# Performance work log

Hardware: AMD Instinct MI355X
Metric: run time of the kernel (lower is better)

## Reference

```python
import jax, jax.numpy as jnp
import numpy as np

H = 8  # attention_heads


def _ln(x, w, b, eps=1e-5):
    mu = x.mean(axis=-1, keepdims=True)
    var = x.var(axis=-1, keepdims=True)
    return (x - mu) / jnp.sqrt(var + eps) * w + b


def setup_inputs() -> dict:
    key = jax.random.key(0)
    ks = jax.random.split(key, 10)
    B, T, C, U, D, P = 4, 256, 2048, 4, 512, 512
    s = 0.02
    inp = {
        "model_embed": jax.random.normal(ks[0], (B, T, D), jnp.float32),
        "context_embed_key": jax.random.normal(ks[1], (C, U, D), jnp.float32),
        "context_embed_value": jax.random.normal(ks[2], (C, D), jnp.float32),
        "ln1_w": jnp.ones((D,), jnp.float32), "ln1_b": jnp.zeros((D,), jnp.float32),
        "ln2_w": jnp.ones((D,), jnp.float32), "ln2_b": jnp.zeros((D,), jnp.float32),
        "ln3_w": jnp.ones((D,), jnp.float32), "ln3_b": jnp.zeros((D,), jnp.float32),
        "ln4_w": jnp.ones((D,), jnp.float32), "ln4_b": jnp.zeros((D,), jnp.float32),
        "wq": jax.random.normal(ks[3], (D, D), jnp.float32) * s, "bq": jnp.zeros((D,), jnp.float32),
        "wk": jax.random.normal(ks[4], (D, D), jnp.float32) * s, "bk": jnp.zeros((D,), jnp.float32),
        "wv": jax.random.normal(ks[5], (D, D), jnp.float32) * s, "bv": jnp.zeros((D,), jnp.float32),
        "wo": jax.random.normal(ks[6], (D, D), jnp.float32) * s, "bo": jnp.zeros((D,), jnp.float32),
        "wp": jax.random.normal(ks[7], (D, P), jnp.float32) * s, "bp": jnp.zeros((P,), jnp.float32),
    }
    return inp


def reference(model_embed, context_embed_key, context_embed_value,
              ln1_w, ln1_b, ln2_w, ln2_b, ln3_w, ln3_b, ln4_w, ln4_b,
              wq, bq, wk, bk, wv, bv, wo, bo, wp, bp):
    B, T, D = model_embed.shape
    C, U, _ = context_embed_key.shape
    dk = D // H
    # pre-attention LayerNorms (norm_before_x1/x2/x3)
    q = _ln(model_embed, ln1_w, ln1_b)
    k = _ln(context_embed_key, ln2_w, ln2_b)
    v = _ln(context_embed_value, ln3_w, ln3_b)
    # q/k/v projections, split heads
    q = (q @ wq + bq).reshape(B, T, H, dk)
    k = (k @ wk + bk).reshape(C, U, H, dk)
    v = (v @ wv + bv).reshape(C, H, dk)
    # ColBERT late interaction: score every query token against every
    # context vector, MaxSim over the U vectors of each context entry.
    scores = jnp.einsum('bthd,cuhd->bhtcu', q, k) / jnp.sqrt(jnp.asarray(dk, q.dtype))
    scores = scores.max(axis=-1)                 # [B,H,T,C]
    attn = jax.nn.softmax(scores, axis=-1)       # softmax over contexts C
    out = jnp.einsum('bhtc,chd->bthd', attn, v).reshape(B, T, D)
    out = out @ wo + bo                          # attention output proj
    out = _ln(out, ln4_w, ln4_b)                 # norm_after
    return out @ wp + bp                         # final proj -> [B,T,P]
```

## Files before the change

kernel.cpp:

```cpp
#include <hip/hip_runtime.h>
#include <hip/hip_bf16.h>

using bf16 = __hip_bfloat16;

#define D_DIM 512
#define C_DIM 2048
#define U_DIM 4
#define DK 64

typedef __attribute__((ext_vector_type(8))) short short8;
typedef __attribute__((ext_vector_type(8))) unsigned short ushort8;
typedef __attribute__((ext_vector_type(4))) float f32x4;

__device__ __forceinline__ float dload(const void* p, size_t i, int f) {
    return f ? ((const float*)p)[i] : __bfloat162float(((const bf16*)p)[i]);
}
__device__ __forceinline__ unsigned f2bf(float x) {
    bf16 b = __float2bfloat16(x);
    return (unsigned)*(unsigned short*)&b;
}
__device__ __forceinline__ float bf2f(unsigned short us) {
    unsigned u = ((unsigned)us) << 16;
    return __builtin_bit_cast(float, u);
}

__device__ __forceinline__ int block_detect(const void* __restrict__ x) {
    __shared__ int sred[4];
    const bf16* xb = (const bf16*)x;
    int tid = threadIdx.x;
    int cnt = 0;
    #pragma unroll
    for (int i = 0; i < 4; ++i) {
        ushort8 a = *(const ushort8*)(xb + (size_t)(i * 256 + tid) * 8);
        #pragma unroll
        for (int j = 0; j < 8; ++j) {
            float v = fabsf(bf2f(a[j]));
            if (!(v <= 100.0f)) cnt++;
        }
    }
    #pragma unroll
    for (int o = 32; o > 0; o >>= 1) cnt += __shfl_down(cnt, o);
    if ((tid & 63) == 0) sred[tid >> 6] = cnt;
    __syncthreads();
    int c = sred[0] + sred[1] + sred[2] + sred[3];
    return (c > 400) ? 1 : 0;
}

template <bool LN, bool XF, bool WF>
__device__ __forceinline__ void pack_a_body(const void* __restrict__ X,
                                            const void* __restrict__ lnw,
                                            const void* __restrict__ lnb,
                                            uint4* __restrict__ Af, int tt) {
    int m = threadIdx.x >> 4;
    int kbL = threadIdx.x & 15;
    int row = tt * 16 + m;
    float v[32];
    float s = 0.0f, ss = 0.0f;
    #pragma unroll
    for (int i = 0; i < 4; ++i) {
        int k0 = (kbL + i * 16) * 8;
        if constexpr (XF) {
            const float4* p = (const float4*)((const float*)X + (size_t)row * D_DIM + k0);
            float4 a = p[0], b = p[1];
            v[i*8+0] = a.x; v[i*8+1] = a.y; v[i*8+2] = a.z; v[i*8+3] = a.w;
            v[i*8+4] = b.x; v[i*8+5] = b.y; v[i*8+6] = b.z; v[i*8+7] = b.w;
        } else {
            ushort8 a = *(const ushort8*)((const bf16*)X + (size_t)row * D_DIM + k0);
            #pragma unroll
            for (int j = 0; j < 8; ++j) v[i*8+j] = bf2f(a[j]);
        }
        #pragma unroll
        for (int j = 0; j < 8; ++j) { float x = v[i*8+j]; s += x; ss += x * x; }
    }
    float mu = 0.0f, rs = 1.0f;
    if (LN) {
        #pragma unroll
        for (int o = 1; o < 16; o <<= 1) { s += __shfl_xor(s, o); ss += __shfl_xor(ss, o); }
        mu = s * (1.0f / D_DIM);
        float var = ss * (1.0f / D_DIM) - mu * mu;
        rs = rsqrtf(var + 1e-5f);
    }
    #pragma unroll
    for (int i = 0; i < 4; ++i) {
        int kb = kbL + i * 16;
        int k0 = kb * 8;
        float lw[8], lb[8];
        if (LN) {
            if constexpr (WF) {
                const float4* pw = (const float4*)((const float*)lnw + k0);
                const float4* pb = (const float4*)((const float*)lnb + k0);
                float4 w0 = pw[0], w1 = pw[1], b0 = pb[0], b1 = pb[1];
                lw[0]=w0.x; lw[1]=w0.y; lw[2]=w0.z; lw[3]=w0.w;
                lw[4]=w1.x; lw[5]=w1.y; lw[6]=w1.z; lw[7]=w1.w;
                lb[0]=b0.x; lb[1]=b0.y; lb[2]=b0.z; lb[3]=b0.w;
                lb[4]=b1.x; lb[5]=b1.y; lb[6]=b1.z; lb[7]=b1.w;
            } else {
                ushort8 w8 = *(const ushort8*)((const bf16*)lnw + k0);
                ushort8 b8 = *(const ushort8*)((const bf16*)lnb + k0);
                #pragma unroll
                for (int j = 0; j < 8; ++j) { lw[j] = bf2f(w8[j]); lb[j] = bf2f(b8[j]); }
            }
        }
        unsigned pk[4];
        #pragma unroll
        for (int jp = 0; jp < 4; ++jp) {
            float v0 = v[i * 8 + jp * 2];
            float v1 = v[i * 8 + jp * 2 + 1];
            if (LN) {
                v0 = (v0 - mu) * rs * lw[jp * 2] + lb[jp * 2];
                v1 = (v1 - mu) * rs * lw[jp * 2 + 1] + lb[jp * 2 + 1];
            }
            pk[jp] = f2bf(v0) | (f2bf(v1) << 16);
        }
        uint4 wv = {pk[0], pk[1], pk[2], pk[3]};
        Af[((size_t)tt * 64 + kb) * 16 + m] = wv;
    }
}

template <bool WF>
__device__ __forceinline__ void pack_w_body(const void* __restrict__ W,
                                            uint4* __restrict__ Bf, int b,
                                            float (*t)[65]) {
    int n0 = (b & 7) * 64, k0 = (b >> 3) * 64;
    int tid = threadIdx.x;
    if constexpr (WF) {
        #pragma unroll
        for (int i = 0; i < 4; ++i) {
            int e = i * 256 + tid;
            int r = e >> 4, c = (e & 15) * 4;
            float4 a = *(const float4*)((const float*)W + (size_t)(k0 + r) * D_DIM + n0 + c);
            t[r][c] = a.x; t[r][c+1] = a.y; t[r][c+2] = a.z; t[r][c+3] = a.w;
        }
    } else {
        #pragma unroll
        for (int i = 0; i < 2; ++i) {
            int e = i * 256 + tid;
            int r = e >> 3, c = (e & 7) * 8;
            ushort8 a = *(const ushort8*)((const bf16*)W + (size_t)(k0 + r) * D_DIM + n0 + c);
            #pragma unroll
            for (int j = 0; j < 8; ++j) t[r][c + j] = bf2f(a[j]);
        }
    }
    __syncthreads();
    #pragma unroll
    for (int i = 0; i < 2; ++i) {
        int e = i * 256 + tid;
        int nl = e & 63, kbl = e >> 6;
        unsigned pk[4];
        #pragma unroll
        for (int jp = 0; jp < 4; ++jp)
            pk[jp] = f2bf(t[kbl * 8 + jp * 2][nl]) | (f2bf(t[kbl * 8 + jp * 2 + 1][nl]) << 16);
        uint4 wv = {pk[0], pk[1], pk[2], pk[3]};
        int n = n0 + nl;
        Bf[(((size_t)(n >> 4)) * 64 + (k0 / 8 + kbl)) * 16 + (n & 15)] = wv;
    }
}

__global__ __launch_bounds__(256, 1)
void pack_all_kernel(const void* __restrict__ me, const void* __restrict__ l1w, const void* __restrict__ l1b,
                     const void* __restrict__ ck, const void* __restrict__ l2w, const void* __restrict__ l2b,
                     const void* __restrict__ cv, const void* __restrict__ l3w, const void* __restrict__ l3b,
                     uint4* __restrict__ Aq, uint4* __restrict__ Ak, uint4* __restrict__ Av,
                     const void* W0, const void* W1, const void* W2,
                     const void* W3, const void* W4,
                     uint4* B0, uint4* B1, uint4* B2, uint4* B3, uint4* B4,
                     int* __restrict__ flagp) {
    __shared__ float t[64][65];
    int f = block_detect(me);
    if (blockIdx.x == 0 && threadIdx.x == 0) *flagp = f;
    int b = blockIdx.x;
    const void* Ws[5] = {W0, W1, W2, W3, W4};
    uint4* Bs[5] = {B0, B1, B2, B3, B4};
    if (f) {
        if (b < 64)       pack_a_body<true, true, true>(me, l1w, l1b, Aq, b);
        else if (b < 576) pack_a_body<true, true, true>(ck, l2w, l2b, Ak, b - 64);
        else if (b < 704) pack_a_body<true, true, true>(cv, l3w, l3b, Av, b - 576);
        else { int c = b - 704; pack_w_body<true>(Ws[c >> 6], Bs[c >> 6], c & 63, t); }
    } else {
        if (b < 64)       pack_a_body<true, false, false>(me, l1w, l1b, Aq, b);
        else if (b < 576) pack_a_body<true, false, false>(ck, l2w, l2b, Ak, b - 64);
        else if (b < 704) pack_a_body<true, false, false>(cv, l3w, l3b, Av, b - 576);
        else { int c = b - 704; pack_w_body<false>(Ws[c >> 6], Bs[c >> 6], c & 63, t); }
    }
}

template <int OUT>
__device__ __forceinline__ void mfma_gemm_body(const uint4* __restrict__ Af,
                                               const uint4* __restrict__ Bf,
                                               const void* __restrict__ bias,
                                               uint4* __restrict__ Fout, int Rtt,
                                               int f, int bx, int by,
                                               float (*t)[65]) {
    int w = threadIdx.x >> 6, lane = threadIdx.x & 63;
    int q = lane >> 4, mn = lane & 15;
    int mt = by * 4 + w;
    int nt0 = bx * 4;
    f32x4 acc[4] = {{0.f,0.f,0.f,0.f},{0.f,0.f,0.f,0.f},{0.f,0.f,0.f,0.f},{0.f,0.f,0.f,0.f}};
    for (int kw = 0; kw < 16; ++kw) {
        short8 a = *(const short8*)(Af + ((size_t)mt * 64 + kw * 4 + q) * 16 + mn);
        #pragma unroll
        for (int i = 0; i < 4; ++i) {
            short8 b = *(const short8*)(Bf + (((size_t)(nt0 + i)) * 64 + kw * 4 + q) * 16 + mn);
            acc[i] = __builtin_amdgcn_mfma_f32_16x16x32_bf16(a, b, acc[i], 0, 0, 0);
        }
    }
    #pragma unroll
    for (int i = 0; i < 4; ++i) {
        float bv = dload(bias, (nt0 + i) * 16 + mn, f);
        #pragma unroll
        for (int r = 0; r < 4; ++r)
            t[w * 16 + q * 4 + r][i * 16 + mn] = acc[i][r] + bv;
    }
    __syncthreads();
    int h = bx;
    if constexpr (OUT == 1) {
        #pragma unroll
        for (int e0 = 0; e0 < 2; ++e0) {
            int e = e0 * 256 + threadIdx.x;
            int m = e & 15, kb = (e >> 4) & 7, ttl = e >> 7;
            const float* src = &t[ttl * 16 + m][kb * 8];
            uint4 wv;
            wv.x = f2bf(src[0]) | (f2bf(src[1]) << 16);
            wv.y = f2bf(src[2]) | (f2bf(src[3]) << 16);
            wv.z = f2bf(src[4]) | (f2bf(src[5]) << 16);
            wv.w = f2bf(src[6]) | (f2bf(src[7]) << 16);
            Fout[(((size_t)h * Rtt + by * 4 + ttl) * 8 + kb) * 16 + m] = wv;
        }
    } else if constexpr (OUT == 2) {
        #pragma unroll
        for (int e0 = 0; e0 < 2; ++e0) {
            int e = e0 * 256 + threadIdx.x;
            int lane2 = e & 63, nt = (e >> 6) & 3, ctl = e >> 8;
            int nm2 = lane2 & 15, q2 = lane2 >> 4;
            int col = nt * 16 + nm2;
            int rb = ctl * 32 + q2 * 8;
            uint4 wv;
            wv.x = f2bf(t[rb + 0][col]) | (f2bf(t[rb + 1][col]) << 16);
            wv.y = f2bf(t[rb + 2][col]) | (f2bf(t[rb + 3][col]) << 16);
            wv.z = f2bf(t[rb + 4][col]) | (f2bf(t[rb + 5][col]) << 16);
            wv.w = f2bf(t[rb + 6][col]) | (f2bf(t[rb + 7][col]) << 16);
            Fout[(((size_t)h * 64 + by * 2 + ctl) * 4 + nt) * 64 + lane2] = wv;
        }
    } else {
        #pragma unroll
        for (int e0 = 0; e0 < 2; ++e0) {
            int e = e0 * 256 + threadIdx.x;
            int m2 = e & 15, kb = (e >> 4) & 7, u = e >> 7;
            const float* src = &t[m2 * 4 + u][kb * 8];
            uint4 wv;
            wv.x = f2bf(src[0]) | (f2bf(src[1]) << 16);
            wv.y = f2bf(src[2]) | (f2bf(src[3]) << 16);
            wv.z = f2bf(src[4]) | (f2bf(src[5]) << 16);
            wv.w = f2bf(src[6]) | (f2bf(src[7]) << 16);
            int nt = by * 4 + u;
            Fout[(((size_t)h * 512 + nt) * 8 + kb) * 16 + m2] = wv;
        }
    }
}

__global__ __launch_bounds__(256, 2)
void gemm_qkv_kernel(const uint4* __restrict__ Aq, const uint4* __restrict__ Ak,
                     const uint4* __restrict__ Av,
                     const uint4* __restrict__ wfq, const uint4* __restrict__ wfk,
                     const uint4* __restrict__ wfv,
                     const void* __restrict__ bq, const void* __restrict__ bk,
                     const void* __restrict__ bv,
                     uint4* __restrict__ qf, uint4* __restrict__ kf,
                     uint4* __restrict__ vf,
                     const int* __restrict__ flagp) {
    __shared__ float t[64][65];
    int f = *flagp;
    int b = blockIdx.x;
    if (b < 1024) {
        mfma_gemm_body<3>(Ak, wfk, bk, kf, 512, f, b >> 7, b & 127, t);
    } else if (b < 1280) {
        int c = b - 1024;
        mfma_gemm_body<2>(Av, wfv, bv, vf, 0, f, c >> 5, c & 31, t);
    } else {
        int c = b - 1280;
        mfma_gemm_body<1>(Aq, wfq, bq, qf, 64, f, c >> 4, c & 15, t);
    }
}

__global__ __launch_bounds__(512, 1)
void attn_fused_kernel(const uint4* __restrict__ qf, const uint4* __restrict__ kf,
                       const uint4* __restrict__ vf, uint4* __restrict__ oAf) {
    __shared__ float sp[8][16][36];
    __shared__ float opar[8][16][64];
    __shared__ float mpar[8][16];
    __shared__ float lpar[8][16];
    int tid = threadIdx.x;
    int w = tid >> 6, lane = tid & 63;
    int q = lane >> 4, nm = lane & 15;
    int b = blockIdx.x;
    int h = b & 7;
    int rt = b >> 3;
    int s = w;

    short8 a0 = *(const short8*)(qf + (((size_t)h * 64 + rt) * 8 + q) * 16 + nm);
    short8 a1 = *(const short8*)(qf + (((size_t)h * 64 + rt) * 8 + 4 + q) * 16 + nm);

    f32x4 sc[8][2];
    #pragma unroll
    for (int st = 0; st < 8; ++st) {
        #pragma unroll
        for (int hh = 0; hh < 2; ++hh) {
            int ct16 = (s * 8 + st) * 2 + hh;
            f32x4 scv = {-1e30f, -1e30f, -1e30f, -1e30f};
            __builtin_amdgcn_s_setprio(1);
            #pragma unroll
            for (int u = 0; u < 4; ++u) {
                int nt = ct16 * 4 + u;
                short8 b0 = *(const short8*)(kf + (((size_t)h * 512 + nt) * 8 + q) * 16 + nm);
                short8 b1 = *(const short8*)(kf + (((size_t)h * 512 + nt) * 8 + 4 + q) * 16 + nm);
                f32x4 acc = {0.0f, 0.0f, 0.0f, 0.0f};
                acc = __builtin_amdgcn_mfma_f32_16x16x32_bf16(a0, b0, acc, 0, 0, 0);
                acc = __builtin_amdgcn_mfma_f32_16x16x32_bf16(a1, b1, acc, 0, 0, 0);
                #pragma unroll
                for (int r = 0; r < 4; ++r) scv[r] = fmaxf(scv[r], acc[r]);
            }
            __builtin_amdgcn_s_setprio(0);
            #pragma unroll
            for (int r = 0; r < 4; ++r) sc[st][hh][r] = scv[r] * 0.125f;
        }
    }

    float mrow[4], lrow[4];
    #pragma unroll
    for (int r = 0; r < 4; ++r) {
        float m = sc[0][0][r];
        #pragma unroll
        for (int st = 0; st < 8; ++st) {
            m = fmaxf(m, sc[st][0][r]);
            m = fmaxf(m, sc[st][1][r]);
        }
        m = fmaxf(m, __shfl_xor(m, 1));
        m = fmaxf(m, __shfl_xor(m, 2));
        m = fmaxf(m, __shfl_xor(m, 4));
        m = fmaxf(m, __shfl_xor(m, 8));
        mrow[r] = m;
        lrow[r] = 0.0f;
    }

    f32x4 acc_o[4] = {{0.f,0.f,0.f,0.f},{0.f,0.f,0.f,0.f},{0.f,0.f,0.f,0.f},{0.f,0.f,0.f,0.f}};
    #pragma unroll
    for (int st = 0; st < 8; ++st) {
        #pragma unroll
        for (int r = 0; r < 4; ++r) {
            float p0 = __expf(sc[st][0][r] - mrow[r]);
            float p1 = __expf(sc[st][1][r] - mrow[r]);
            sp[w][q * 4 + r][nm] = p0;
            sp[w][q * 4 + r][16 + nm] = p1;
            lrow[r] += p0 + p1;
        }
        float4 pa0 = *(const float4*)&sp[w][nm][q * 8];
        float4 pa1 = *(const float4*)&sp[w][nm][q * 8 + 4];
        uint4 av;
        av.x = f2bf(pa0.x) | (f2bf(pa0.y) << 16);
        av.y = f2bf(pa0.z) | (f2bf(pa0.w) << 16);
        av.z = f2bf(pa1.x) | (f2bf(pa1.y) << 16);
        av.w = f2bf(pa1.z) | (f2bf(pa1.w) << 16);
        short8 ap = *(short8*)&av;
        int ct32 = s * 8 + st;
        __builtin_amdgcn_s_setprio(1);
        #pragma unroll
        for (int nt2 = 0; nt2 < 4; ++nt2) {
            short8 bv = *(const short8*)(vf + (((size_t)h * 64 + ct32) * 4 + nt2) * 64 + lane);
            acc_o[nt2] = __builtin_amdgcn_mfma_f32_16x16x32_bf16(ap, bv, acc_o[nt2], 0, 0, 0);
        }
        __builtin_amdgcn_s_setprio(0);
    }

    #pragma unroll
    for (int r = 0; r < 4; ++r) {
        float ps = lrow[r];
        ps += __shfl_xor(ps, 1);
        ps += __shfl_xor(ps, 2);
        ps += __shfl_xor(ps, 4);
        ps += __shfl_xor(ps, 8);
        lrow[r] = ps;
    }

    #pragma unroll
    for (int nt2 = 0; nt2 < 4; ++nt2)
        #pragma unroll
        for (int r = 0; r < 4; ++r)
            opar[w][q * 4 + r][nt2 * 16 + nm] = acc_o[nt2][r];
    if (nm == 0) {
        #pragma unroll
        for (int r = 0; r < 4; ++r) {
            mpar[w][q * 4 + r] = mrow[r];
            lpar[w][q * 4 + r] = lrow[r];
        }
    }
    __syncthreads();

    if (tid < 128) {
        int row = tid & 15, dg = tid >> 4;
        float M = -1e30f;
        #pragma unroll
        for (int ss = 0; ss < 8; ++ss) M = fmaxf(M, mpar[ss][row]);
        float L = 0.0f;
        float o[8] = {0.f,0.f,0.f,0.f,0.f,0.f,0.f,0.f};
        #pragma unroll
        for (int ss = 0; ss < 8; ++ss) {
            float e = __expf(mpar[ss][row] - M);
            L += lpar[ss][row] * e;
            const float* po = &opar[ss][row][dg * 8];
            #pragma unroll
            for (int j = 0; j < 8; ++j) o[j] += po[j] * e;
        }
        float inv = 1.0f / L;
        uint4 u;
        u.x = f2bf(o[0] * inv) | (f2bf(o[1] * inv) << 16);
        u.y = f2bf(o[2] * inv) | (f2bf(o[3] * inv) << 16);
        u.z = f2bf(o[4] * inv) | (f2bf(o[5] * inv) << 16);
        u.w = f2bf(o[6] * inv) | (f2bf(o[7] * inv) << 16);
        int kb = h * 8 + dg;
        oAf[((size_t)rt * 64 + kb) * 16 + row] = u;
    }
}

__global__ __launch_bounds__(512, 1)
void tail2_kernel(const uint4* __restrict__ oAf,
                  const uint4* __restrict__ wfo, const uint4* __restrict__ wfp,
                  const void* __restrict__ bo, const void* __restrict__ bp,
                  const void* __restrict__ ln4w, const void* __restrict__ ln4b,
                  float* __restrict__ Y, const int* __restrict__ flagp) {
    __shared__ uint4 lfr[64][16];
    __shared__ float xs[8][16][68];
    __shared__ float lw4[512], lb4[512];
    __shared__ float sred[8][16][2];
    int f = *flagp;
    int tid = threadIdx.x;
    int rt = blockIdx.x;
    if (tid < 512) { lw4[tid] = dload(ln4w, tid, f); lb4[tid] = dload(ln4b, tid, f); }

    int w = tid >> 6, lane = tid & 63;
    int q = lane >> 4, mn = lane & 15;

    f32x4 acc[4] = {{0.f,0.f,0.f,0.f},{0.f,0.f,0.f,0.f},{0.f,0.f,0.f,0.f},{0.f,0.f,0.f,0.f}};
    for (int kw = 0; kw < 16; ++kw) {
        short8 a = *(const short8*)(oAf + ((size_t)rt * 64 + kw * 4 + q) * 16 + mn);
        #pragma unroll
        for (int i = 0; i < 4; ++i) {
            int nt = w * 4 + i;
            short8 b = *(const short8*)(wfo + ((size_t)nt * 64 + kw * 4 + q) * 16 + mn);
            acc[i] = __builtin_amdgcn_mfma_f32_16x16x32_bf16(a, b, acc[i], 0, 0, 0);
        }
    }
    #pragma unroll
    for (int i = 0; i < 4; ++i) {
        float bv = dload(bo, (w * 4 + i) * 16 + mn, f);
        #pragma unroll
        for (int r = 0; r < 4; ++r) acc[i][r] += bv;
    }

    {
        float ps[4], pq[4];
        #pragma unroll
        for (int r = 0; r < 4; ++r) {
            float s = 0.f, sq = 0.f;
            #pragma unroll
            for (int i = 0; i < 4; ++i) { float x = acc[i][r]; s += x; sq += x * x; }
            #pragma unroll
            for (int o = 1; o < 16; o <<= 1) { s += __shfl_xor(s, o); sq += __shfl_xor(sq, o); }
            ps[r] = s; pq[r] = sq;
        }
        if (mn == 0) {
            #pragma unroll
            for (int r = 0; r < 4; ++r) { sred[w][q*4+r][0] = ps[r]; sred[w][q*4+r][1] = pq[r]; }
        }
    }
    __syncthreads();

    float mu[4], rs[4];
    #pragma unroll
    for (int r = 0; r < 4; ++r) {
        int rr = q * 4 + r;
        float s = 0.f, sq = 0.f;
        #pragma unroll
        for (int ww = 0; ww < 8; ++ww) { s += sred[ww][rr][0]; sq += sred[ww][rr][1]; }
        mu[r] = s * (1.0f / D_DIM);
        float var = sq * (1.0f / D_DIM) - mu[r] * mu[r];
        rs[r] = rsqrtf(var + 1e-5f);
    }

    #pragma unroll
    for (int i = 0; i < 4; ++i) {
        int col = w * 64 + i * 16 + mn;
        float g = lw4[col], bb = lb4[col];
        #pragma unroll
        for (int r = 0; r < 4; ++r) {
            float x = (acc[i][r] - mu[r]) * rs[r] * g + bb;
            xs[w][q * 4 + r][i * 16 + mn] = x;
        }
    }
    __syncthreads();

    #pragma unroll
    for (int it = 0; it < 2; ++it) {
        int idx = it * 64 + lane;
        int m = idx & 15, kbl = idx >> 4;
        const float* src = &xs[w][m][kbl * 8];
        float4 s0 = *(const float4*)src;
        float4 s1 = *(const float4*)(src + 4);
        uint4 u;
        u.x = f2bf(s0.x) | (f2bf(s0.y) << 16);
        u.y = f2bf(s0.z) | (f2bf(s0.w) << 16);
        u.z = f2bf(s1.x) | (f2bf(s1.y) << 16);
        u.w = f2bf(s1.z) | (f2bf(s1.w) << 16);
        lfr[w * 8 + kbl][m] = u;
    }
    __syncthreads();

    f32x4 acc2[4] = {{0.f,0.f,0.f,0.f},{0.f,0.f,0.f,0.f},{0.f,0.f,0.f,0.f},{0.f,0.f,0.f,0.f}};
    for (int kw = 0; kw < 16; ++kw) {
        short8 a = *(const short8*)&lfr[kw * 4 + q][mn];
        #pragma unroll
        for (int i = 0; i < 4; ++i) {
            int nt = w * 4 + i;
            short8 b = *(const short8*)(wfp + ((size_t)nt * 64 + kw * 4 + q) * 16 + mn);
            acc2[i] = __builtin_amdgcn_mfma_f32_16x16x32_bf16(a, b, acc2[i], 0, 0, 0);
        }
    }
    #pragma unroll
    for (int i = 0; i < 4; ++i) {
        int col = (w * 4 + i) * 16 + mn;
        float bv = dload(bp, col, f);
        #pragma unroll
        for (int r = 0; r < 4; ++r)
            Y[(size_t)(rt * 16 + q * 4 + r) * D_DIM + col] = acc2[i][r] + bv;
    }
}

extern "C" void kernel_launch(void* const* d_in, const int* in_sizes, int n_in,
                              void* d_out, int out_size, void* d_ws, size_t ws_size,
                              hipStream_t stream) {
    const void* model_embed = d_in[0];
    const void* ctx_key     = d_in[1];
    const void* ctx_val     = d_in[2];
    const void* ln1w = d_in[3];  const void* ln1b = d_in[4];
    const void* ln2w = d_in[5];  const void* ln2b = d_in[6];
    const void* ln3w = d_in[7];  const void* ln3b = d_in[8];
    const void* ln4w = d_in[9];  const void* ln4b = d_in[10];
    const void* wq = d_in[11];   const void* bq = d_in[12];
    const void* wk = d_in[13];   const void* bk = d_in[14];
    const void* wv = d_in[15];   const void* bv = d_in[16];
    const void* wo = d_in[17];   const void* bo = d_in[18];
    const void* wp = d_in[19];   const void* bp = d_in[20];

    int*   flagp = (int*)d_ws;
    float* ws    = (float*)d_ws + 16;
    float* o1    = ws;
    float* qTf   = o1 + 524288;
    float* kTf   = qTf + 262144;
    float* Aqf   = kTf + 2097152;
    float* Akf   = Aqf + 262144;
    float* Avf   = Akf + 2097152;
    float* vff   = Avf + 524288;
    float* wfr   = vff + 524288;

    uint4* qf  = (uint4*)qTf;
    uint4* kf  = (uint4*)kTf;
    uint4* Aq  = (uint4*)Aqf;
    uint4* Ak  = (uint4*)Akf;
    uint4* Av  = (uint4*)Avf;
    uint4* vf  = (uint4*)vff;
    uint4* oAf = (uint4*)o1;
    uint4* wfq = (uint4*)wfr;
    uint4* wfk = wfq + 32768;
    uint4* wfv = wfk + 32768;
    uint4* wfo = wfv + 32768;
    uint4* wfp = wfo + 32768;

    pack_all_kernel<<<1024, 256, 0, stream>>>(model_embed, ln1w, ln1b,
                                              ctx_key, ln2w, ln2b,
                                              ctx_val, ln3w, ln3b,
                                              Aq, Ak, Av,
                                              wq, wk, wv, wo, wp,
                                              wfq, wfk, wfv, wfo, wfp, flagp);

    gemm_qkv_kernel<<<1408, 256, 0, stream>>>(Aq, Ak, Av, wfq, wfk, wfv,
                                              bq, bk, bv, qf, kf, vf, flagp);

    attn_fused_kernel<<<512, 512, 0, stream>>>(qf, kf, vf, oAf);

    tail2_kernel<<<64, 512, 0, stream>>>(oAf, wfo, wfp, bo, bp,
                                         ln4w, ln4b, (float*)d_out, flagp);

    (void)ws_size;
}
```

Baseline: 182.2 us.

## Split tail kernel into two launches to spread output projection and LN over more blocks

The fused tail kernel (output projection, LayerNorm, final projection) ran on only 64 blocks of 512 threads. It becomes two kernels of 256 blocks each, with each block handling a quarter of the columns. The first kernel writes the fp32 projection and per-quarter row sum/sumsq partials to workspace. The second combines the partials, applies LN while converting A fragments to bf16 on the fly, and runs the final projection. This fills more of the GPU's compute units but adds a kernel launch and a global round trip for the intermediate activations.

```diff
diff --git a/kernel.cpp b/kernel.cpp
--- a/kernel.cpp
+++ b/kernel.cpp
@@ -421,48 +421,50 @@
     }
 }
 
-__global__ __launch_bounds__(512, 1)
-void tail2_kernel(const uint4* __restrict__ oAf,
-                  const uint4* __restrict__ wfo, const uint4* __restrict__ wfp,
-                  const void* __restrict__ bo, const void* __restrict__ bp,
-                  const void* __restrict__ ln4w, const void* __restrict__ ln4b,
-                  float* __restrict__ Y, const int* __restrict__ flagp) {
-    __shared__ uint4 lfr[64][16];
-    __shared__ float xs[8][16][68];
-    __shared__ float lw4[512], lb4[512];
-    __shared__ float sred[8][16][2];
+__global__ __launch_bounds__(256, 1)
+void tailA_kernel(const uint4* __restrict__ oAf, const uint4* __restrict__ wfo,
+                  const void* __restrict__ bo,
+                  float* __restrict__ xg, float* __restrict__ stats4,
+                  const int* __restrict__ flagp) {
+    __shared__ float sred[4][16][2];
     int f = *flagp;
     int tid = threadIdx.x;
-    int rt = blockIdx.x;
-    if (tid < 512) { lw4[tid] = dload(ln4w, tid, f); lb4[tid] = dload(ln4b, tid, f); }
-
+    int b = blockIdx.x;
+    int rt = b >> 2, cq = b & 3;
     int w = tid >> 6, lane = tid & 63;
     int q = lane >> 4, mn = lane & 15;
-
-    f32x4 acc[4] = {{0.f,0.f,0.f,0.f},{0.f,0.f,0.f,0.f},{0.f,0.f,0.f,0.f},{0.f,0.f,0.f,0.f}};
+    int nt0 = cq * 8 + w * 2;
+
+    f32x4 acc[2] = {{0.f,0.f,0.f,0.f},{0.f,0.f,0.f,0.f}};
     for (int kw = 0; kw < 16; ++kw) {
         short8 a = *(const short8*)(oAf + ((size_t)rt * 64 + kw * 4 + q) * 16 + mn);
         #pragma unroll
-        for (int i = 0; i < 4; ++i) {
-            int nt = w * 4 + i;
-            short8 b = *(const short8*)(wfo + ((size_t)nt * 64 + kw * 4 + q) * 16 + mn);
-            acc[i] = __builtin_amdgcn_mfma_f32_16x16x32_bf16(a, b, acc[i], 0, 0, 0);
-        }
-    }
-    #pragma unroll
-    for (int i = 0; i < 4; ++i) {
-        float bv = dload(bo, (w * 4 + i) * 16 + mn, f);
+        for (int i = 0; i < 2; ++i) {
+            short8 bb = *(const short8*)(wfo + ((size_t)(nt0 + i) * 64 + kw * 4 + q) * 16 + mn);
+            acc[i] = __builtin_amdgcn_mfma_f32_16x16x32_bf16(a, bb, acc[i], 0, 0, 0);
+        }
+    }
+    #pragma unroll
+    for (int i = 0; i < 2; ++i) {
+        float bv = dload(bo, (nt0 + i) * 16 + mn, f);
         #pragma unroll
         for (int r = 0; r < 4; ++r) acc[i][r] += bv;
+    }
+
+    #pragma unroll
+    for (int i = 0; i < 2; ++i) {
+        int col = (nt0 + i) * 16 + mn;
+        #pragma unroll
+        for (int r = 0; r < 4; ++r)
+            xg[(size_t)(rt * 16 + q * 4 + r) * D_DIM + col] = acc[i][r];
     }
 
     {
         float ps[4], pq[4];
         #pragma unroll
         for (int r = 0; r < 4; ++r) {
-            float s = 0.f, sq = 0.f;
-            #pragma unroll
-            for (int i = 0; i < 4; ++i) { float x = acc[i][r]; s += x; sq += x * x; }
+            float s = acc[0][r] + acc[1][r];
+            float sq = acc[0][r] * acc[0][r] + acc[1][r] * acc[1][r];
             #pragma unroll
             for (int o = 1; o < 16; o <<= 1) { s += __shfl_xor(s, o); sq += __shfl_xor(sq, o); }
             ps[r] = s; pq[r] = sq;
@@ -473,64 +475,71 @@
         }
     }
     __syncthreads();
-
-    float mu[4], rs[4];
-    #pragma unroll
-    for (int r = 0; r < 4; ++r) {
-        int rr = q * 4 + r;
-        float s = 0.f, sq = 0.f;
-        #pragma unroll
-        for (int ww = 0; ww < 8; ++ww) { s += sred[ww][rr][0]; sq += sred[ww][rr][1]; }
-        mu[r] = s * (1.0f / D_DIM);
-        float var = sq * (1.0f / D_DIM) - mu[r] * mu[r];
-        rs[r] = rsqrtf(var + 1e-5f);
-    }
-
-    #pragma unroll
-    for (int i = 0; i < 4; ++i) {
-        int col = w * 64 + i * 16 + mn;
-        float g = lw4[col], bb = lb4[col];
-        #pragma unroll
-        for (int r = 0; r < 4; ++r) {
-            float x = (acc[i][r] - mu[r]) * rs[r] * g + bb;
-            xs[w][q * 4 + r][i * 16 + mn] = x;
-        }
+    if (tid < 32) {
+        int row = tid & 15, which = tid >> 4;
+        float v = sred[0][row][which] + sred[1][row][which] +
+                  sred[2][row][which] + sred[3][row][which];
+        stats4[((size_t)(rt * 16 + row) * 4 + cq) * 2 + which] = v;
+    }
+}
+
+__global__ __launch_bounds__(256, 1)
+void tailB_kernel(const float* __restrict__ xg, const float* __restrict__ stats4,
+                  const uint4* __restrict__ wfp, const void* __restrict__ bp,
+                  const void* __restrict__ ln4w, const void* __restrict__ ln4b,
+                  float* __restrict__ Y, const int* __restrict__ flagp) {
+    __shared__ float lw4[512], lb4[512];
+    __shared__ float smu[16], srs[16];
+    int f = *flagp;
+    int tid = threadIdx.x;
+    int b = blockIdx.x;
+    int rt = b >> 2, cq = b & 3;
+    for (int i = tid; i < 512; i += 256) { lw4[i] = dload(ln4w, i, f); lb4[i] = dload(ln4b, i, f); }
+    if (tid < 16) {
+        const float* sp4 = stats4 + (size_t)(rt * 16 + tid) * 8;
+        float s  = ((sp4[0] + sp4[2]) + sp4[4]) + sp4[6];
+        float sq = ((sp4[1] + sp4[3]) + sp4[5]) + sp4[7];
+        float mu = s * (1.0f / D_DIM);
+        float var = sq * (1.0f / D_DIM) - mu * mu;
+        smu[tid] = mu;
+        srs[tid] = rsqrtf(var + 1e-5f);
     }
     __syncthreads();
 
-    #pragma unroll
-    for (int it = 0; it < 2; ++it) {
-        int idx = it * 64 + lane;
-        int m = idx & 15, kbl = idx >> 4;
-        const float* src = &xs[w][m][kbl * 8];
-        float4 s0 = *(const float4*)src;
-        float4 s1 = *(const float4*)(src + 4);
-        uint4 u;
-        u.x = f2bf(s0.x) | (f2bf(s0.y) << 16);
-        u.y = f2bf(s0.z) | (f2bf(s0.w) << 16);
-        u.z = f2bf(s1.x) | (f2bf(s1.y) << 16);
-        u.w = f2bf(s1.z) | (f2bf(s1.w) << 16);
-        lfr[w * 8 + kbl][m] = u;
-    }
-    __syncthreads();
-
-    f32x4 acc2[4] = {{0.f,0.f,0.f,0.f},{0.f,0.f,0.f,0.f},{0.f,0.f,0.f,0.f},{0.f,0.f,0.f,0.f}};
+    int w = tid >> 6, lane = tid & 63;
+    int q = lane >> 4, mn = lane & 15;
+    int nt0 = cq * 8 + w * 2;
+    float mu = smu[mn], rs = srs[mn];
+    const float* xrow = xg + (size_t)(rt * 16 + mn) * D_DIM;
+
+    f32x4 acc[2] = {{0.f,0.f,0.f,0.f},{0.f,0.f,0.f,0.f}};
     for (int kw = 0; kw < 16; ++kw) {
-        short8 a = *(const short8*)&lfr[kw * 4 + q][mn];
-        #pragma unroll
-        for (int i = 0; i < 4; ++i) {
-            int nt = w * 4 + i;
-            short8 b = *(const short8*)(wfp + ((size_t)nt * 64 + kw * 4 + q) * 16 + mn);
-            acc2[i] = __builtin_amdgcn_mfma_f32_16x16x32_bf16(a, b, acc2[i], 0, 0, 0);
-        }
-    }
-    #pragma unroll
-    for (int i = 0; i < 4; ++i) {
-        int col = (w * 4 + i) * 16 + mn;
+        int k0 = (kw * 4 + q) * 8;
+        float4 x0 = *(const float4*)(xrow + k0);
+        float4 x1 = *(const float4*)(xrow + k0 + 4);
+        float e[8] = {x0.x, x0.y, x0.z, x0.w, x1.x, x1.y, x1.z, x1.w};
+        unsigned pk[4];
+        #pragma unroll
+        for (int jp = 0; jp < 4; ++jp) {
+            float v0 = (e[jp*2]   - mu) * rs * lw4[k0 + jp*2]   + lb4[k0 + jp*2];
+            float v1 = (e[jp*2+1] - mu) * rs * lw4[k0 + jp*2+1] + lb4[k0 + jp*2+1];
+            pk[jp] = f2bf(v0) | (f2bf(v1) << 16);
+        }
+        uint4 av = {pk[0], pk[1], pk[2], pk[3]};
+        short8 a = *(short8*)&av;
+        #pragma unroll
+        for (int i = 0; i < 2; ++i) {
+            short8 bb = *(const short8*)(wfp + ((size_t)(nt0 + i) * 64 + kw * 4 + q) * 16 + mn);
+            acc[i] = __builtin_amdgcn_mfma_f32_16x16x32_bf16(a, bb, acc[i], 0, 0, 0);
+        }
+    }
+    #pragma unroll
+    for (int i = 0; i < 2; ++i) {
+        int col = (nt0 + i) * 16 + mn;
         float bv = dload(bp, col, f);
         #pragma unroll
         for (int r = 0; r < 4; ++r)
-            Y[(size_t)(rt * 16 + q * 4 + r) * D_DIM + col] = acc2[i][r] + bv;
+            Y[(size_t)(rt * 16 + q * 4 + r) * D_DIM + col] = acc[i][r] + bv;
     }
 }
 
@@ -560,6 +569,8 @@
     float* Avf   = Akf + 2097152;
     float* vff   = Avf + 524288;
     float* wfr   = vff + 524288;
+    float* xg    = wfr + 655360;
+    float* st4   = xg + 524288;
 
     uint4* qf  = (uint4*)qTf;
     uint4* kf  = (uint4*)kTf;
@@ -586,8 +597,10 @@
 
     attn_fused_kernel<<<512, 512, 0, stream>>>(qf, kf, vf, oAf);
 
-    tail2_kernel<<<64, 512, 0, stream>>>(oAf, wfo, wfp, bo, bp,
-                                         ln4w, ln4b, (float*)d_out, flagp);
+    tailA_kernel<<<256, 256, 0, stream>>>(oAf, wfo, bo, xg, st4, flagp);
+
+    tailB_kernel<<<256, 256, 0, stream>>>(xg, st4, wfp, bp, ln4w, ln4b,
+                                          (float*)d_out, flagp);
 
     (void)ws_size;
 }
```

Result: slower. 186.3 us (+2.2%).

## Stage GEMM B fragments through double-buffered shared memory in QKV projection

Applied to the files above, without the earlier changes.

The QKV GEMM body now loads the weight (B) fragments cooperatively into a double-buffered LDS tile. The next K-chunk is prefetched into registers while MFMAs run on the current chunk. Previously each of the four waves read the same B fragments from global memory on its own, so this is meant to cut redundant global/L2 traffic and hide load latency. The cost is 32 KB of extra LDS per block, which may lower occupancy, plus extra barriers.

```diff
diff --git a/kernel.cpp b/kernel.cpp
--- a/kernel.cpp
+++ b/kernel.cpp
@@ -190,20 +190,54 @@
                                                const void* __restrict__ bias,
                                                uint4* __restrict__ Fout, int Rtt,
                                                int f, int bx, int by,
-                                               float (*t)[65]) {
-    int w = threadIdx.x >> 6, lane = threadIdx.x & 63;
+                                               float (*t)[65],
+                                               uint4 (*bbuf)[1024]) {
+    int tid = threadIdx.x;
+    int w = tid >> 6, lane = tid & 63;
     int q = lane >> 4, mn = lane & 15;
     int mt = by * 4 + w;
     int nt0 = bx * 4;
+
+    uint4 stg[4];
+    #pragma unroll
+    for (int j = 0; j < 4; ++j) {
+        int e = j * 256 + tid;
+        int emn = e & 15, rest = e >> 4, i = rest & 3, kq = rest >> 2;
+        stg[j] = Bf[(((size_t)(nt0 + i)) * 64 + kq) * 16 + emn];
+    }
+    #pragma unroll
+    for (int j = 0; j < 4; ++j) bbuf[0][j * 256 + tid] = stg[j];
+    __syncthreads();
+
     f32x4 acc[4] = {{0.f,0.f,0.f,0.f},{0.f,0.f,0.f,0.f},{0.f,0.f,0.f,0.f},{0.f,0.f,0.f,0.f}};
-    for (int kw = 0; kw < 16; ++kw) {
-        short8 a = *(const short8*)(Af + ((size_t)mt * 64 + kw * 4 + q) * 16 + mn);
-        #pragma unroll
-        for (int i = 0; i < 4; ++i) {
-            short8 b = *(const short8*)(Bf + (((size_t)(nt0 + i)) * 64 + kw * 4 + q) * 16 + mn);
-            acc[i] = __builtin_amdgcn_mfma_f32_16x16x32_bf16(a, b, acc[i], 0, 0, 0);
-        }
-    }
+    #pragma unroll
+    for (int p = 0; p < 4; ++p) {
+        const int cur = p & 1;
+        if (p < 3) {
+            #pragma unroll
+            for (int j = 0; j < 4; ++j) {
+                int e = j * 256 + tid;
+                int emn = e & 15, rest = e >> 4, i = rest & 3, kq = rest >> 2;
+                stg[j] = Bf[(((size_t)(nt0 + i)) * 64 + (p + 1) * 16 + kq) * 16 + emn];
+            }
+        }
+        #pragma unroll
+        for (int kwl = 0; kwl < 4; ++kwl) {
+            int kw = p * 4 + kwl;
+            short8 a = *(const short8*)(Af + ((size_t)mt * 64 + kw * 4 + q) * 16 + mn);
+            #pragma unroll
+            for (int i = 0; i < 4; ++i) {
+                short8 b = *(const short8*)&bbuf[cur][((kwl * 4 + q) * 4 + i) * 16 + mn];
+                acc[i] = __builtin_amdgcn_mfma_f32_16x16x32_bf16(a, b, acc[i], 0, 0, 0);
+            }
+        }
+        if (p < 3) {
+            #pragma unroll
+            for (int j = 0; j < 4; ++j) bbuf[cur ^ 1][j * 256 + tid] = stg[j];
+            __syncthreads();
+        }
+    }
+
     #pragma unroll
     for (int i = 0; i < 4; ++i) {
         float bv = dload(bias, (nt0 + i) * 16 + mn, f);
@@ -269,16 +303,17 @@
                      uint4* __restrict__ vf,
                      const int* __restrict__ flagp) {
     __shared__ float t[64][65];
+    __shared__ uint4 bbuf[2][1024];
     int f = *flagp;
     int b = blockIdx.x;
     if (b < 1024) {
-        mfma_gemm_body<3>(Ak, wfk, bk, kf, 512, f, b >> 7, b & 127, t);
+        mfma_gemm_body<3>(Ak, wfk, bk, kf, 512, f, b >> 7, b & 127, t, bbuf);
     } else if (b < 1280) {
         int c = b - 1024;
-        mfma_gemm_body<2>(Av, wfv, bv, vf, 0, f, c >> 5, c & 31, t);
+        mfma_gemm_body<2>(Av, wfv, bv, vf, 0, f, c >> 5, c & 31, t, bbuf);
     } else {
         int c = b - 1280;
-        mfma_gemm_body<1>(Aq, wfq, bq, qf, 64, f, c >> 4, c & 15, t);
+        mfma_gemm_body<1>(Aq, wfq, bq, qf, 64, f, c >> 4, c & 15, t, bbuf);
     }
 }
 
```

Result: faster. 175.6 us (-3.6%).
